# Performance work log

Hardware: AMD Instinct MI355X
Metric: run time of the kernel (lower is better)

## Reference

```python
import jax, jax.numpy as jnp
import numpy as np


def setup_inputs() -> dict:
    key = jax.random.key(0)
    k1, k2, k3, k4 = jax.random.split(key, 4)
    B, Tv, Ta, D = 8, 2048, 2048, 256
    return {
        "visual_features": jax.random.normal(k1, (B, Tv, D), dtype=jnp.float32),
        "audio_features": jax.random.normal(k2, (B, Ta, D), dtype=jnp.float32),
        "visual_weights": jax.random.uniform(k3, (D, D), dtype=jnp.float32),
        "audio_weights": jax.random.uniform(k4, (D, D), dtype=jnp.float32),
        "num_neighbors": 8,
    }


def _pairwise_l2(vm, am):
    # ||v - a|| via the expanded form to avoid the [B,Tv,Ta,D] intermediate.
    sq = (
        jnp.sum(vm * vm, -1)[:, :, None]
        + jnp.sum(am * am, -1)[:, None, :]
        - 2.0 * jnp.einsum("btd,bsd->bts", vm, am)
    )
    sq = jnp.maximum(sq, 0.0)
    # safe sqrt: subgradient 0 at 0 (matches torch.norm backward convention)
    return jnp.where(sq > 0, jnp.sqrt(jnp.where(sq > 0, sq, 1.0)), 0.0)


def reference(visual_features, audio_features, visual_weights, audio_weights, num_neighbors):
    vm = visual_features @ visual_weights  # [B,Tv,D]
    am = audio_features @ audio_weights    # [B,Ta,D]
    graph = jnp.exp(-_pairwise_l2(vm, am))  # [B,Tv,Ta]
    # topk over the visual axis (dim=1): move it last for lax.top_k
    _, idx = jax.lax.top_k(jnp.swapaxes(graph, 1, 2), num_neighbors)  # [B,Ta,k]
    idx = jnp.swapaxes(idx, 1, 2)  # [B,k,Ta]
    # broadcasted gather along axis 1: result [B,k,Ta,D]
    vn = jnp.take_along_axis(visual_features[:, :, None, :], idx[..., None], axis=1)
    an = jnp.take_along_axis(audio_features[:, :, None, :], idx[..., None], axis=1)
    # mean over dim=2 (the Ta axis of the gathered neighbors) -> [B,k,D]
    return vn.mean(axis=2), an.mean(axis=2)
```

## Files before the change

kernel.cpp:

```cpp
#include <hip/hip_runtime.h>
#include <cstddef>
#include <cstdint>

namespace {
constexpr int kB   = 8;
constexpr int kT   = 2048;
constexpr int kD   = 256;
constexpr int kK   = 8;
constexpr int kM   = kB * kT;
constexpr int kNC  = kB * kT;
constexpr int kColCap = 64;
constexpr int kOvCap  = 1 << 17;
constexpr int kStr = 264;
constexpr float kMinNormalF = 1.17549435e-38f;
}

typedef __attribute__((ext_vector_type(8)))  __bf16 bf16x8;
typedef __attribute__((ext_vector_type(16))) float  f32x16;

__device__ inline unsigned short f2bf_rne(float x) {
  unsigned u = __float_as_uint(x);
  unsigned r = (u + 0x7FFFu + ((u >> 16) & 1u)) >> 16;
  return (unsigned short)r;
}
__device__ inline float bf2f(unsigned short h) {
  return __uint_as_float((unsigned)h << 16);
}
union FragU { uint4 u4; bf16x8 v; };

__device__ inline void async16(const unsigned short* g, unsigned short* l) {
  __builtin_amdgcn_global_load_lds(
      (const __attribute__((address_space(1))) unsigned int*)(const void*)g,
      (__attribute__((address_space(3))) unsigned int*)(void*)l, 16, 0, 0);
}

__device__ inline void stage_tile_async(const unsigned short* src,
                                        unsigned short* S, int w, int lane) {
  const int hi = lane >> 5, lo = lane & 31;
#pragma unroll
  for (int i = 0; i < 8; ++i) {
    const int p = w * 8 + i;
    const int rowl = p * 2 + hi;
    const int c = lo ^ (rowl & 31);
    async16(src + (size_t)rowl * kD + c * 8, S + p * 512);
  }
}
__device__ inline uint4 lds_frag(const unsigned short* S, int row, int kc, int half) {
  const int c = (kc * 2 + half) ^ (row & 31);
  return *reinterpret_cast<const uint4*>(S + row * 256 + c * 8);
}

__global__ __launch_bounds__(256) void prep(const float* __restrict__ W0,
                                            const float* __restrict__ W1,
                                            unsigned short* __restrict__ T0,
                                            unsigned short* __restrict__ T1,
                                            unsigned* __restrict__ zeroBase,
                                            int zeroWords,
                                            unsigned* __restrict__ outW) {
  const int blk = blockIdx.x;
  if (blk < 128) {
    const float* W = (blk & 64) ? W1 : W0;
    unsigned short* WT = (blk & 64) ? T1 : T0;
    const int t = blk & 63;
    const int c0 = (t & 7) * 32, k0 = (t >> 3) * 32;
    __shared__ float tile[32][33];
    const int tx = threadIdx.x & 31, ty = threadIdx.x >> 5;
#pragma unroll
    for (int i = 0; i < 4; ++i)
      tile[ty + i * 8][tx] = W[(size_t)(k0 + ty + i * 8) * kD + c0 + tx];
    __syncthreads();
#pragma unroll
    for (int i = 0; i < 4; ++i)
      WT[(size_t)(c0 + ty + i * 8) * kD + k0 + tx] = f2bf_rne(tile[tx][ty + i * 8]);
  } else {
    for (int i = (blk - 128) * 256 + threadIdx.x; i < zeroWords; i += 32 * 256)
      zeroBase[i] = 0u;
    for (int i = (blk - 128) * 256 + threadIdx.x; i < 2 * kB * kK * kD; i += 32 * 256)
      outW[i] = 0u;
  }
}

__global__ __launch_bounds__(256) void gemm_hyb(const float* __restrict__ Xv,
                                                const float* __restrict__ Xa,
                                                const unsigned short* __restrict__ WvT,
                                                const unsigned short* __restrict__ WaT,
                                                unsigned short* __restrict__ Cv,
                                                unsigned short* __restrict__ Ca,
                                                float* __restrict__ nv,
                                                float* __restrict__ na) {
  __shared__ unsigned short S[64 * kStr + 64 * 256];
  unsigned short* bufA = S;
  unsigned short* bufB = S + 64 * kStr;
  const int z = blockIdx.z;
  const float* X = z ? Xa : Xv;
  const unsigned short* WT = z ? WaT : WvT;
  unsigned short* Cb = z ? Ca : Cv;
  float* nrm = z ? na : nv;
  const int r0 = blockIdx.x * 64;
  const int tid = threadIdx.x;
  const int w = tid >> 6, lane = tid & 63;
  const int wt = w & 1, wc = w >> 1;
  const int half = lane >> 5, ln = lane & 31;

#pragma unroll
  for (int i = 0; i < 16; ++i) {
    const int idx = i * 256 + tid;
    const int row = idx >> 6, g = idx & 63;
    const float4 v = *reinterpret_cast<const float4*>(X + (size_t)(r0 + row) * kD + g * 4);
    ushort4 o;
    o.x = f2bf_rne(v.x); o.y = f2bf_rne(v.y); o.z = f2bf_rne(v.z); o.w = f2bf_rne(v.w);
    *reinterpret_cast<ushort4*>(bufA + row * kStr + g * 4) = o;
  }
  __syncthreads();

  stage_tile_async(WT, bufB, w, lane);
  uint4 afr[16];
#pragma unroll
  for (int kc = 0; kc < 16; ++kc)
    afr[kc] = *reinterpret_cast<const uint4*>(bufA + (wt * 32 + ln) * kStr + kc * 16 + half * 8);
  __syncthreads();

  float ns[16];
#pragma unroll
  for (int r = 0; r < 16; ++r) ns[r] = 0.0f;

  for (int ct = 0; ct < 4; ++ct) {
    unsigned short* cur = (ct & 1) ? bufA : bufB;
    unsigned short* nxt = (ct & 1) ? bufB : bufA;
    if (ct < 3)
      stage_tile_async(WT + (size_t)(ct + 1) * 64 * kD, nxt, w, lane);
    const int c0 = ct * 64;
    f32x16 acc;
#pragma unroll
    for (int i = 0; i < 16; ++i) acc[i] = 0.0f;
#pragma unroll
    for (int kc = 0; kc < 16; ++kc) {
      FragU fa, fb;
      fa.u4 = afr[kc];
      fb.u4 = lds_frag(cur, wc * 32 + ln, kc, half);
      acc = __builtin_amdgcn_mfma_f32_32x32x16_bf16(fa.v, fb.v, acc, 0, 0, 0);
    }
    const int col = c0 + wc * 32 + ln;
#pragma unroll
    for (int r = 0; r < 16; ++r) {
      const int row = r0 + wt * 32 + (r & 3) + 8 * (r >> 2) + 4 * half;
      const unsigned short us = f2bf_rne(acc[r]);
      Cb[(size_t)row * kD + col] = us;
      const float f = bf2f(us);
      ns[r] += f * f;
    }
    if (ct < 3) __syncthreads();
  }
#pragma unroll
  for (int r = 0; r < 16; ++r) {
    float v = ns[r];
#pragma unroll
    for (int off = 1; off < 32; off <<= 1) v += __shfl_xor(v, off, 64);
    if (ln == 0) {
      const int row = r0 + wt * 32 + (r & 3) + 8 * (r >> 2) + 4 * half;
      atomicAdd(nrm + row, v);
    }
  }
}

__global__ __launch_bounds__(256) void keys_v15(const unsigned short* __restrict__ vmb,
                                                const unsigned short* __restrict__ amb,
                                                const float* __restrict__ vn2,
                                                const float* __restrict__ an2,
                                                unsigned* __restrict__ colCount,
                                                uint2* __restrict__ colRecs,
                                                unsigned* __restrict__ ovCount,
                                                uint2* __restrict__ ovRecs) {
  __shared__ unsigned short S[2][64 * 256];
  const int hw = blockIdx.x + (blockIdx.y << 4) + (blockIdx.z << 7);
  const int lg = ((hw & 7) << 7) | (hw >> 3);
  const int b = lg >> 7;
  const int t0 = (lg & 15) << 7;
  const int sr0 = ((lg >> 4) & 7) << 8;
  const int tid = threadIdx.x;
  const int w = tid >> 6, lane = tid & 63;
  const int half = lane >> 5, ln = lane & 31;

  stage_tile_async(vmb + ((size_t)b * kT + t0) * kD, S[0], w, lane);
  stage_tile_async(vmb + ((size_t)b * kT + t0 + 64) * kD, S[1], w, lane);
  __syncthreads();
  uint4 afr[16];
  {
    const unsigned short* Sa = S[w >> 1];
#pragma unroll
    for (int kc = 0; kc < 16; ++kc)
      afr[kc] = lds_frag(Sa, (w & 1) * 32 + ln, kc, half);
  }
  __syncthreads();

  stage_tile_async(amb + ((size_t)b * kT + sr0) * kD, S[0], w, lane);
  __syncthreads();

  const float* v2p = vn2 + (size_t)b * kT + t0 + w * 32;

  for (int st = 0; st < 4; ++st) {
    const int s0 = sr0 + st * 64;
    const int cur = st & 1;
    if (st < 3)
      stage_tile_async(amb + ((size_t)b * kT + s0 + 64) * kD, S[cur ^ 1], w, lane);
    f32x16 acc[2];
#pragma unroll
    for (int j = 0; j < 2; ++j)
#pragma unroll
      for (int i = 0; i < 16; ++i) acc[j][i] = 0.0f;
#pragma unroll
    for (int kc = 0; kc < 16; ++kc) {
      FragU fa; fa.u4 = afr[kc];
#pragma unroll
      for (int ss = 0; ss < 2; ++ss) {
        FragU fb;
        fb.u4 = lds_frag(S[cur], ss * 32 + ln, kc, half);
        acc[ss] = __builtin_amdgcn_mfma_f32_32x32x16_bf16(fa.v, fb.v, acc[ss], 0, 0, 0);
      }
    }
    float a2s[2];
#pragma unroll
    for (int ss = 0; ss < 2; ++ss)
      a2s[ss] = an2[(size_t)b * kT + s0 + ss * 32 + ln];
#pragma unroll
    for (int g = 0; g < 4; ++g) {
      const float4 v2 = *reinterpret_cast<const float4*>(v2p + g * 8 + half * 4);
      const float v2a[4] = {v2.x, v2.y, v2.z, v2.w};
#pragma unroll
      for (int ss = 0; ss < 2; ++ss) {
        const int s = s0 + ss * 32 + ln;
        const float a2 = a2s[ss];
        const int c = (b << 11) | s;
#pragma unroll
        for (int q = 0; q < 4; ++q) {
          const float raw = v2a[q] + a2 - 2.0f * acc[ss][4 * g + q];
          if (raw < 7744.0f) {
            const float dist = sqrtf(fmaxf(raw, 0.0f));
            const float e = expf(-dist);
            if (e >= kMinNormalF) {
              const int t = t0 + w * 32 + g * 8 + half * 4 + q;
              const unsigned slot = atomicAdd(&colCount[c], 1u);
              if (slot < (unsigned)kColCap) {
                colRecs[(size_t)c * kColCap + slot] = make_uint2(__float_as_uint(e), (unsigned)t);
              } else {
                const unsigned pos = ((unsigned)b << 22) | ((unsigned)s << 11) | (unsigned)t;
                const unsigned oi = atomicAdd(ovCount, 1u);
                if (oi < (unsigned)kOvCap) ovRecs[oi] = make_uint2(__float_as_uint(e), pos);
              }
            }
          }
        }
      }
    }
    if (st < 3) __syncthreads();
  }
}

__global__ __launch_bounds__(256) void gather_fused(const float* __restrict__ visual,
                                                    const float* __restrict__ audio,
                                                    const unsigned* __restrict__ colCount,
                                                    const uint2* __restrict__ colRecs,
                                                    const unsigned* __restrict__ ovCount,
                                                    const uint2* __restrict__ ovRecs,
                                                    float* __restrict__ out) {
  __shared__ int sIdx[32];
  const int u = blockIdx.x;
  const int bj = u >> 6, ch = u & 63;
  const int b = bj >> 3, j = bj & 7;
  const int tid = threadIdx.x;
  if (tid < 32) {
    const int s = ch * 32 + tid;
    const int c = (b << 11) | s;
    unsigned K[8]; int T[8];
#pragma unroll
    for (int i = 0; i < 8; ++i) { K[i] = 0u; T[i] = 0x7FFFFFFF; }
    const int cnt = (int)colCount[c];
    const int m = min(cnt, kColCap);
    for (int i = 0; i < m; ++i) {
      const uint2 r = colRecs[(size_t)c * kColCap + i];
      const unsigned kx = r.x; const int tx = (int)r.y;
      if (kx > K[7] || (kx == K[7] && tx < T[7])) {
        K[7] = kx; T[7] = tx;
#pragma unroll
        for (int q = 7; q >= 1; --q) {
          const bool sw = (K[q] > K[q - 1]) || (K[q] == K[q - 1] && T[q] < T[q - 1]);
          if (sw) {
            const unsigned tk = K[q]; K[q] = K[q - 1]; K[q - 1] = tk;
            const int tt = T[q];      T[q] = T[q - 1]; T[q - 1] = tt;
          }
        }
      }
    }
    if (cnt > kColCap) {
      int n = (int)*ovCount;
      if (n > kOvCap) n = kOvCap;
      for (int i = 0; i < n; ++i) {
        const uint2 r = ovRecs[i];
        if ((int)(r.y >> 11) == c) {
          const unsigned kx = r.x; const int tx = (int)(r.y & 2047u);
          if (kx > K[7] || (kx == K[7] && tx < T[7])) {
            K[7] = kx; T[7] = tx;
#pragma unroll
            for (int q = 7; q >= 1; --q) {
              const bool sw = (K[q] > K[q - 1]) || (K[q] == K[q - 1] && T[q] < T[q - 1]);
              if (sw) {
                const unsigned tk = K[q]; K[q] = K[q - 1]; K[q - 1] = tk;
                const int tt = T[q];      T[q] = T[q - 1]; T[q - 1] = tt;
              }
            }
          }
        }
      }
    }
    int mcnt = 0;
#pragma unroll
    for (int i = 0; i < 8; ++i) if (K[i] > 0u) mcnt++;
    int outv[8];
#pragma unroll
    for (int i = 0; i < 8; ++i) outv[i] = T[i];
    int cand = 0;
    for (int r = mcnt; r < 8; ++r) {
      bool taken = true;
      while (taken) {
        taken = false;
#pragma unroll
        for (int q = 0; q < 8; ++q)
          if (q < mcnt && T[q] == cand) taken = true;
        if (taken) cand++;
      }
      outv[r] = cand++;
    }
    sIdx[tid] = outv[j];
  }
  __syncthreads();
  float accV = 0.f, accA = 0.f;
  for (int i = 0; i < 32; ++i) {
    const int t = sIdx[i];
    const size_t base = ((size_t)b * kT + t) * kD + tid;
    accV += visual[base];
    accA += audio[base];
  }
  atomicAdd(&out[(size_t)bj * kD + tid], accV * (1.0f / kT));
  atomicAdd(&out[(size_t)kB * kK * kD + (size_t)bj * kD + tid], accA * (1.0f / kT));
}

extern "C" void kernel_launch(void* const* d_in, const int* in_sizes, int n_in,
                              void* d_out, int out_size, void* d_ws, size_t ws_size,
                              hipStream_t stream) {
  (void)in_sizes; (void)n_in; (void)out_size; (void)ws_size;
  const float* visual = (const float*)d_in[0];
  const float* audio  = (const float*)d_in[1];
  const float* Wv     = (const float*)d_in[2];
  const float* Wa     = (const float*)d_in[3];
  float* out = (float*)d_out;

  char* ws = (char*)d_ws;
  unsigned short* WvT = (unsigned short*)ws;
  unsigned short* WaT = WvT + (size_t)kD * kD;
  unsigned short* vmb = WaT + (size_t)kD * kD;
  unsigned short* amb = vmb + (size_t)kM * kD;
  float* vn2 = (float*)(amb + (size_t)kM * kD);
  float* an2 = vn2 + kM;
  unsigned* colCount = (unsigned*)(an2 + kM);
  unsigned* ovCount  = colCount + kNC;
  uint2* colRecs = (uint2*)(ovCount + 8);
  uint2* ovRecs  = colRecs + (size_t)kNC * kColCap;
  const int zeroWords = 2 * kM + kNC + 8;

  prep<<<dim3(160), 256, 0, stream>>>(Wv, Wa, WvT, WaT, (unsigned*)vn2, zeroWords,
                                      (unsigned*)out);
  gemm_hyb<<<dim3(kM / 64, 1, 2), 256, 0, stream>>>(visual, audio, WvT, WaT,
                                                    vmb, amb, vn2, an2);
  keys_v15<<<dim3(kT / 128, kT / 256, kB), 256, 0, stream>>>(vmb, amb, vn2, an2,
                                                             colCount, colRecs, ovCount, ovRecs);
  gather_fused<<<dim3(4096), 256, 0, stream>>>(visual, audio, colCount, colRecs,
                                               ovCount, ovRecs, out);
}
```

Measured before the change: 150.1 us.

## Single-buffer LDS in keys kernel and raise occupancy with launch bounds

Cuts the keys kernel's LDS from two 64x256 bf16 tiles to one and adds a min-blocks hint of 4 per CU. The visual A-fragments are staged in two sequential passes through the single buffer. The MFMA accumulation over the two audio sub-tiles is reordered so only one 32x32 accumulator is live at a time, which lowers register pressure. In exchange it drops the double-buffered prefetch of the next audio tile, so loads are no longer overlapped with compute inside a block and the kernel relies on other resident blocks to hide latency.

```diff
diff --git a/kernel.cpp b/kernel.cpp
--- a/kernel.cpp
+++ b/kernel.cpp
@@ -163,15 +163,15 @@
   }
 }
 
-__global__ __launch_bounds__(256) void keys_v15(const unsigned short* __restrict__ vmb,
-                                                const unsigned short* __restrict__ amb,
-                                                const float* __restrict__ vn2,
-                                                const float* __restrict__ an2,
-                                                unsigned* __restrict__ colCount,
-                                                uint2* __restrict__ colRecs,
-                                                unsigned* __restrict__ ovCount,
-                                                uint2* __restrict__ ovRecs) {
-  __shared__ unsigned short S[2][64 * 256];
+__global__ __launch_bounds__(256, 4) void keys_v16(const unsigned short* __restrict__ vmb,
+                                                   const unsigned short* __restrict__ amb,
+                                                   const float* __restrict__ vn2,
+                                                   const float* __restrict__ an2,
+                                                   unsigned* __restrict__ colCount,
+                                                   uint2* __restrict__ colRecs,
+                                                   unsigned* __restrict__ ovCount,
+                                                   uint2* __restrict__ ovRecs) {
+  __shared__ unsigned short S[64 * 256];
   const int hw = blockIdx.x + (blockIdx.y << 4) + (blockIdx.z << 7);
   const int lg = ((hw & 7) << 7) | (hw >> 3);
   const int b = lg >> 7;
@@ -181,59 +181,48 @@
   const int w = tid >> 6, lane = tid & 63;
   const int half = lane >> 5, ln = lane & 31;
 
-  stage_tile_async(vmb + ((size_t)b * kT + t0) * kD, S[0], w, lane);
-  stage_tile_async(vmb + ((size_t)b * kT + t0 + 64) * kD, S[1], w, lane);
-  __syncthreads();
   uint4 afr[16];
-  {
-    const unsigned short* Sa = S[w >> 1];
-#pragma unroll
-    for (int kc = 0; kc < 16; ++kc)
-      afr[kc] = lds_frag(Sa, (w & 1) * 32 + ln, kc, half);
-  }
-  __syncthreads();
-
-  stage_tile_async(amb + ((size_t)b * kT + sr0) * kD, S[0], w, lane);
-  __syncthreads();
+#pragma unroll
+  for (int h = 0; h < 2; ++h) {
+    __syncthreads();
+    stage_tile_async(vmb + ((size_t)b * kT + t0 + h * 64) * kD, S, w, lane);
+    __syncthreads();
+    if ((w >> 1) == h) {
+#pragma unroll
+      for (int kc = 0; kc < 16; ++kc)
+        afr[kc] = lds_frag(S, (w & 1) * 32 + ln, kc, half);
+    }
+  }
 
   const float* v2p = vn2 + (size_t)b * kT + t0 + w * 32;
 
   for (int st = 0; st < 4; ++st) {
     const int s0 = sr0 + st * 64;
-    const int cur = st & 1;
-    if (st < 3)
-      stage_tile_async(amb + ((size_t)b * kT + s0 + 64) * kD, S[cur ^ 1], w, lane);
-    f32x16 acc[2];
-#pragma unroll
-    for (int j = 0; j < 2; ++j)
-#pragma unroll
-      for (int i = 0; i < 16; ++i) acc[j][i] = 0.0f;
-#pragma unroll
-    for (int kc = 0; kc < 16; ++kc) {
-      FragU fa; fa.u4 = afr[kc];
-#pragma unroll
-      for (int ss = 0; ss < 2; ++ss) {
-        FragU fb;
-        fb.u4 = lds_frag(S[cur], ss * 32 + ln, kc, half);
-        acc[ss] = __builtin_amdgcn_mfma_f32_32x32x16_bf16(fa.v, fb.v, acc[ss], 0, 0, 0);
-      }
-    }
-    float a2s[2];
-#pragma unroll
-    for (int ss = 0; ss < 2; ++ss)
-      a2s[ss] = an2[(size_t)b * kT + s0 + ss * 32 + ln];
-#pragma unroll
-    for (int g = 0; g < 4; ++g) {
-      const float4 v2 = *reinterpret_cast<const float4*>(v2p + g * 8 + half * 4);
-      const float v2a[4] = {v2.x, v2.y, v2.z, v2.w};
-#pragma unroll
-      for (int ss = 0; ss < 2; ++ss) {
-        const int s = s0 + ss * 32 + ln;
-        const float a2 = a2s[ss];
-        const int c = (b << 11) | s;
+    __syncthreads();
+    stage_tile_async(amb + ((size_t)b * kT + s0) * kD, S, w, lane);
+    __syncthreads();
+#pragma unroll
+    for (int ss = 0; ss < 2; ++ss) {
+      f32x16 acc;
+#pragma unroll
+      for (int i = 0; i < 16; ++i) acc[i] = 0.0f;
+#pragma unroll
+      for (int kc = 0; kc < 16; ++kc) {
+        FragU fa, fb;
+        fa.u4 = afr[kc];
+        fb.u4 = lds_frag(S, ss * 32 + ln, kc, half);
+        acc = __builtin_amdgcn_mfma_f32_32x32x16_bf16(fa.v, fb.v, acc, 0, 0, 0);
+      }
+      const int s = s0 + ss * 32 + ln;
+      const float a2 = an2[(size_t)b * kT + s];
+      const int c = (b << 11) | s;
+#pragma unroll
+      for (int g = 0; g < 4; ++g) {
+        const float4 v2 = *reinterpret_cast<const float4*>(v2p + g * 8 + half * 4);
+        const float v2a[4] = {v2.x, v2.y, v2.z, v2.w};
 #pragma unroll
         for (int q = 0; q < 4; ++q) {
-          const float raw = v2a[q] + a2 - 2.0f * acc[ss][4 * g + q];
+          const float raw = v2a[q] + a2 - 2.0f * acc[4 * g + q];
           if (raw < 7744.0f) {
             const float dist = sqrtf(fmaxf(raw, 0.0f));
             const float e = expf(-dist);
@@ -252,7 +241,6 @@
         }
       }
     }
-    if (st < 3) __syncthreads();
   }
 }
 
@@ -371,7 +359,7 @@
                                       (unsigned*)out);
   gemm_hyb<<<dim3(kM / 64, 1, 2), 256, 0, stream>>>(visual, audio, WvT, WaT,
                                                     vmb, amb, vn2, an2);
-  keys_v15<<<dim3(kT / 128, kT / 256, kB), 256, 0, stream>>>(vmb, amb, vn2, an2,
+  keys_v16<<<dim3(kT / 128, kT / 256, kB), 256, 0, stream>>>(vmb, amb, vn2, an2,
                                                              colCount, colRecs, ovCount, ovRecs);
   gather_fused<<<dim3(4096), 256, 0, stream>>>(visual, audio, colCount, colRecs,
                                                ovCount, ovRecs, out);
```

New measurement: 176.1 us. 1.17x slower.

## Replace per-column gather with histogram-weighted sum over visual/audio rows

Applied to the files above, without the earlier changes.

The per-column top-k merge now runs once per audio column in a separate kernel. Each column's selected indices are scattered into a per-(b,t,j) count histogram. A second kernel streams the visual and audio rows once and accumulates count-weighted sums for all 8 neighbor slots, rather than redundantly gathering rows 8× across 4096 blocks. This removes the 8× duplicated top-k work and the random gathers. The cost is an extra launch, a larger zeroed workspace, and histogram atomics.

```diff
diff --git a/kernel.cpp b/kernel.cpp
--- a/kernel.cpp
+++ b/kernel.cpp
@@ -256,92 +256,109 @@
   }
 }
 
-__global__ __launch_bounds__(256) void gather_fused(const float* __restrict__ visual,
-                                                    const float* __restrict__ audio,
-                                                    const unsigned* __restrict__ colCount,
-                                                    const uint2* __restrict__ colRecs,
-                                                    const unsigned* __restrict__ ovCount,
-                                                    const uint2* __restrict__ ovRecs,
-                                                    float* __restrict__ out) {
-  __shared__ int sIdx[32];
-  const int u = blockIdx.x;
-  const int bj = u >> 6, ch = u & 63;
-  const int b = bj >> 3, j = bj & 7;
-  const int tid = threadIdx.x;
-  if (tid < 32) {
-    const int s = ch * 32 + tid;
-    const int c = (b << 11) | s;
-    unsigned K[8]; int T[8];
-#pragma unroll
-    for (int i = 0; i < 8; ++i) { K[i] = 0u; T[i] = 0x7FFFFFFF; }
-    const int cnt = (int)colCount[c];
-    const int m = min(cnt, kColCap);
-    for (int i = 0; i < m; ++i) {
-      const uint2 r = colRecs[(size_t)c * kColCap + i];
-      const unsigned kx = r.x; const int tx = (int)r.y;
-      if (kx > K[7] || (kx == K[7] && tx < T[7])) {
-        K[7] = kx; T[7] = tx;
-#pragma unroll
-        for (int q = 7; q >= 1; --q) {
-          const bool sw = (K[q] > K[q - 1]) || (K[q] == K[q - 1] && T[q] < T[q - 1]);
-          if (sw) {
-            const unsigned tk = K[q]; K[q] = K[q - 1]; K[q - 1] = tk;
-            const int tt = T[q];      T[q] = T[q - 1]; T[q - 1] = tt;
-          }
+__global__ __launch_bounds__(256) void finalize_hist(const unsigned* __restrict__ colCount,
+                                                     const uint2* __restrict__ colRecs,
+                                                     const unsigned* __restrict__ ovCount,
+                                                     const uint2* __restrict__ ovRecs,
+                                                     unsigned* __restrict__ hist) {
+  const int c = blockIdx.x * 256 + threadIdx.x;
+  const int b = c >> 11;
+  unsigned K[8]; int T[8];
+#pragma unroll
+  for (int i = 0; i < 8; ++i) { K[i] = 0u; T[i] = 0x7FFFFFFF; }
+  const int cnt = (int)colCount[c];
+  const int m = min(cnt, kColCap);
+  for (int i = 0; i < m; ++i) {
+    const uint2 r = colRecs[(size_t)c * kColCap + i];
+    const unsigned kx = r.x; const int tx = (int)r.y;
+    if (kx > K[7] || (kx == K[7] && tx < T[7])) {
+      K[7] = kx; T[7] = tx;
+#pragma unroll
+      for (int q = 7; q >= 1; --q) {
+        const bool sw = (K[q] > K[q - 1]) || (K[q] == K[q - 1] && T[q] < T[q - 1]);
+        if (sw) {
+          const unsigned tk = K[q]; K[q] = K[q - 1]; K[q - 1] = tk;
+          const int tt = T[q];      T[q] = T[q - 1]; T[q - 1] = tt;
         }
       }
     }
-    if (cnt > kColCap) {
-      int n = (int)*ovCount;
-      if (n > kOvCap) n = kOvCap;
-      for (int i = 0; i < n; ++i) {
-        const uint2 r = ovRecs[i];
-        if ((int)(r.y >> 11) == c) {
-          const unsigned kx = r.x; const int tx = (int)(r.y & 2047u);
-          if (kx > K[7] || (kx == K[7] && tx < T[7])) {
-            K[7] = kx; T[7] = tx;
-#pragma unroll
-            for (int q = 7; q >= 1; --q) {
-              const bool sw = (K[q] > K[q - 1]) || (K[q] == K[q - 1] && T[q] < T[q - 1]);
-              if (sw) {
-                const unsigned tk = K[q]; K[q] = K[q - 1]; K[q - 1] = tk;
-                const int tt = T[q];      T[q] = T[q - 1]; T[q - 1] = tt;
-              }
+  }
+  if (cnt > kColCap) {
+    int n = (int)*ovCount;
+    if (n > kOvCap) n = kOvCap;
+    for (int i = 0; i < n; ++i) {
+      const uint2 r = ovRecs[i];
+      if ((int)(r.y >> 11) == c) {
+        const unsigned kx = r.x; const int tx = (int)(r.y & 2047u);
+        if (kx > K[7] || (kx == K[7] && tx < T[7])) {
+          K[7] = kx; T[7] = tx;
+#pragma unroll
+          for (int q = 7; q >= 1; --q) {
+            const bool sw = (K[q] > K[q - 1]) || (K[q] == K[q - 1] && T[q] < T[q - 1]);
+            if (sw) {
+              const unsigned tk = K[q]; K[q] = K[q - 1]; K[q - 1] = tk;
+              const int tt = T[q];      T[q] = T[q - 1]; T[q - 1] = tt;
             }
           }
         }
       }
     }
-    int mcnt = 0;
-#pragma unroll
-    for (int i = 0; i < 8; ++i) if (K[i] > 0u) mcnt++;
-    int outv[8];
-#pragma unroll
-    for (int i = 0; i < 8; ++i) outv[i] = T[i];
-    int cand = 0;
-    for (int r = mcnt; r < 8; ++r) {
-      bool taken = true;
-      while (taken) {
-        taken = false;
-#pragma unroll
-        for (int q = 0; q < 8; ++q)
-          if (q < mcnt && T[q] == cand) taken = true;
-        if (taken) cand++;
-      }
-      outv[r] = cand++;
-    }
-    sIdx[tid] = outv[j];
-  }
-  __syncthreads();
-  float accV = 0.f, accA = 0.f;
-  for (int i = 0; i < 32; ++i) {
-    const int t = sIdx[i];
-    const size_t base = ((size_t)b * kT + t) * kD + tid;
-    accV += visual[base];
-    accA += audio[base];
-  }
-  atomicAdd(&out[(size_t)bj * kD + tid], accV * (1.0f / kT));
-  atomicAdd(&out[(size_t)kB * kK * kD + (size_t)bj * kD + tid], accA * (1.0f / kT));
+  }
+  int mcnt = 0;
+#pragma unroll
+  for (int i = 0; i < 8; ++i) if (K[i] > 0u) mcnt++;
+  int outv[8];
+#pragma unroll
+  for (int i = 0; i < 8; ++i) outv[i] = T[i];
+  int cand = 0;
+  for (int r = mcnt; r < 8; ++r) {
+    bool taken = true;
+    while (taken) {
+      taken = false;
+#pragma unroll
+      for (int q = 0; q < 8; ++q)
+        if (q < mcnt && T[q] == cand) taken = true;
+      if (taken) cand++;
+    }
+    outv[r] = cand++;
+  }
+#pragma unroll
+  for (int j = 0; j < 8; ++j)
+    atomicAdd(&hist[(((size_t)b << 11) + (unsigned)outv[j]) * kK + j], 1u);
+}
+
+__global__ __launch_bounds__(256) void wsum(const float* __restrict__ visual,
+                                            const float* __restrict__ audio,
+                                            const unsigned* __restrict__ hist,
+                                            float* __restrict__ out) {
+  __shared__ unsigned hs[64 * kK];
+  const int b = blockIdx.y;
+  const int t0 = blockIdx.x * 64;
+  const int d = threadIdx.x;
+  const size_t hbase = (((size_t)b << 11) + t0) * kK;
+  hs[d] = hist[hbase + d];
+  hs[d + 256] = hist[hbase + d + 256];
+  __syncthreads();
+  float accV[8], accA[8];
+#pragma unroll
+  for (int j = 0; j < 8; ++j) { accV[j] = 0.f; accA[j] = 0.f; }
+  const size_t xbase = ((size_t)b * kT + t0) * kD + d;
+  for (int i = 0; i < 64; ++i) {
+    const float v = visual[xbase + (size_t)i * kD];
+    const float a = audio[xbase + (size_t)i * kD];
+#pragma unroll
+    for (int j = 0; j < 8; ++j) {
+      const float cf = (float)hs[i * kK + j];
+      accV[j] += cf * v;
+      accA[j] += cf * a;
+    }
+  }
+#pragma unroll
+  for (int j = 0; j < 8; ++j) {
+    const size_t bj = (size_t)b * kK + j;
+    atomicAdd(&out[bj * kD + d], accV[j] * (1.0f / kT));
+    atomicAdd(&out[(size_t)kB * kK * kD + bj * kD + d], accA[j] * (1.0f / kT));
+  }
 }
 
 extern "C" void kernel_launch(void* const* d_in, const int* in_sizes, int n_in,
@@ -363,9 +380,10 @@
   float* an2 = vn2 + kM;
   unsigned* colCount = (unsigned*)(an2 + kM);
   unsigned* ovCount  = colCount + kNC;
-  uint2* colRecs = (uint2*)(ovCount + 8);
+  unsigned* hist     = ovCount + 8;
+  uint2* colRecs = (uint2*)(hist + (size_t)kM * kK);
   uint2* ovRecs  = colRecs + (size_t)kNC * kColCap;
-  const int zeroWords = 2 * kM + kNC + 8;
+  const int zeroWords = 2 * kM + kNC + 8 + kM * kK;
 
   prep<<<dim3(160), 256, 0, stream>>>(Wv, Wa, WvT, WaT, (unsigned*)vn2, zeroWords,
                                       (unsigned*)out);
@@ -373,6 +391,7 @@
                                                     vmb, amb, vn2, an2);
   keys_v15<<<dim3(kT / 128, kT / 256, kB), 256, 0, stream>>>(vmb, amb, vn2, an2,
                                                              colCount, colRecs, ovCount, ovRecs);
-  gather_fused<<<dim3(4096), 256, 0, stream>>>(visual, audio, colCount, colRecs,
-                                               ovCount, ovRecs, out);
-}
+  finalize_hist<<<dim3(kNC / 256), 256, 0, stream>>>(colCount, colRecs, ovCount,
+                                                     ovRecs, hist);
+  wsum<<<dim3(kT / 64, kB), 256, 0, stream>>>(visual, audio, hist, out);
+}
```

After: 220.4 us. 46.9% more time.
